# Kernel optimization log

Measured on AMD Instinct MI355X. Metric: run time of the kernel, lower is better.

## Reference

```python
import jax, jax.numpy as jnp
import numpy as np

N, E = 50000, 800000
DIN, DH, DOUT, HEADS = 128, 128, 128, 4
NEG_SLOPE = 0.2
LN_EPS = 1e-5


def setup_inputs() -> dict:
    key = jax.random.key(0)
    ks = jax.random.split(key, 20)
    s = 0.05
    inp = {
        "x": jax.random.normal(ks[0], (N, DIN), jnp.float32),
        "edge_index": jax.random.randint(ks[1], (2, E), 0, N, jnp.int32),
        "W_in": jax.random.normal(ks[2], (DIN, DH), jnp.float32) * s,
        "b_in": jnp.zeros((DH,), jnp.float32),
        # GAT layer 0 (heads=4, concat)
        "W0": jax.random.normal(ks[3], (DH, DH), jnp.float32) * s,
        "as0": jax.random.normal(ks[4], (HEADS, DH // HEADS), jnp.float32) * s,
        "ad0": jax.random.normal(ks[5], (HEADS, DH // HEADS), jnp.float32) * s,
        "b0": jnp.zeros((DH,), jnp.float32),
        # GAT layer 1 (heads=4, concat)
        "W1": jax.random.normal(ks[6], (DH, DH), jnp.float32) * s,
        "as1": jax.random.normal(ks[7], (HEADS, DH // HEADS), jnp.float32) * s,
        "ad1": jax.random.normal(ks[8], (HEADS, DH // HEADS), jnp.float32) * s,
        "b1": jnp.zeros((DH,), jnp.float32),
        # GAT layer 2 (heads=1, no concat)
        "W2": jax.random.normal(ks[9], (DH, DOUT), jnp.float32) * s,
        "as2": jax.random.normal(ks[10], (1, DOUT), jnp.float32) * s,
        "ad2": jax.random.normal(ks[11], (1, DOUT), jnp.float32) * s,
        "b2": jnp.zeros((DOUT,), jnp.float32),
    }
    return inp


def layer_norm(x):
    mu = jnp.mean(x, -1, keepdims=True)
    var = jnp.var(x, -1, keepdims=True)
    return (x - mu) * jax.lax.rsqrt(var + LN_EPS)


def gat_conv(x, src, dst, W, a_src, a_dst, bias, heads, concat):
    # x: [N, D_in]; src/dst include self-loops
    n = x.shape[0]
    c = W.shape[1] // heads
    h = (x @ W).reshape(n, heads, c)                       # [N,H,C]
    al_s = jnp.sum(h * a_src[None], -1)                    # [N,H]
    al_d = jnp.sum(h * a_dst[None], -1)                    # [N,H]
    e = jax.nn.leaky_relu(al_s[src] + al_d[dst], NEG_SLOPE)  # [Etot,H]
    m = jax.ops.segment_max(e, dst, num_segments=n)
    ex = jnp.exp(e - m[dst])
    z = jax.ops.segment_sum(ex, dst, num_segments=n)
    alpha = ex / (z[dst] + 1e-16)                          # [Etot,H]
    out = jax.ops.segment_sum(h[src] * alpha[:, :, None], dst, num_segments=n)  # [N,H,C]
    out = out.reshape(n, heads * c) if concat else jnp.mean(out, 1)
    return out + bias


def reference(x, edge_index, W_in, b_in, W0, as0, ad0, b0,
              W1, as1, ad1, b1, W2, as2, ad2, b2):
    n = x.shape[0]
    loop = jnp.arange(n, dtype=edge_index.dtype)
    src = jnp.concatenate([edge_index[0], loop])  # PyG GATConv adds self-loops
    dst = jnp.concatenate([edge_index[1], loop])

    h = jax.nn.relu(x @ W_in + b_in)  # dropout is identity in eval mode

    res = h
    h = gat_conv(h, src, dst, W0, as0, ad0, b0, HEADS, True)
    h = layer_norm(jax.nn.elu(h) + res)

    res = h
    h = gat_conv(h, src, dst, W1, as1, ad1, b1, HEADS, True)
    h = layer_norm(jax.nn.elu(h) + res)

    h = gat_conv(h, src, dst, W2, as2, ad2, b2, 1, False)
    return layer_norm(h)
```

## Files before the change

### kernel.cpp

```cpp
#include <hip/hip_runtime.h>
#include <hip/hip_bf16.h>

typedef unsigned short ushort_t;
typedef unsigned int uint_t;
typedef __attribute__((ext_vector_type(8))) short short8;
typedef __attribute__((ext_vector_type(4))) float f32x4;

__device__ __forceinline__ ushort_t f2bf(float f) {
    uint_t u = __float_as_uint(f);
    uint_t r = (u + 0x7FFFu + ((u >> 16) & 1u)) >> 16;
    return (ushort_t)r;
}
__device__ __forceinline__ float bf2f_lo(uint_t u) { return __uint_as_float(u << 16); }
__device__ __forceinline__ float bf2f_hi(uint_t u) { return __uint_as_float(u & 0xffff0000u); }
__device__ __forceinline__ float bf2f_hi_fast(uint_t u) { return __uint_as_float(u); }

#define BSH 8
#define BCK 256
#define CSR_CAP 6144

__global__ void prep_kernel(const float* __restrict__ W_in,
                            const float* __restrict__ W0, const float* __restrict__ as0,
                            const float* __restrict__ ad0,
                            const float* __restrict__ W1, const float* __restrict__ as1,
                            const float* __restrict__ ad1,
                            const float* __restrict__ W2, const float* __restrict__ as2,
                            const float* __restrict__ ad2,
                            ushort_t* __restrict__ BfIn, ushort_t* __restrict__ Bf0,
                            ushort_t* __restrict__ Bf1, ushort_t* __restrict__ Bf2,
                            const int* __restrict__ ei, int* __restrict__ gcnt,
                            int E, int N, int NB) {
    __shared__ int hist[256];
    int b = blockIdx.x;
    if (b < 35) {
        const float *W, *a_s, *a_d;
        ushort_t* Bf;
        int H, NT, nt;
        if (b < 8)       { W = W_in; a_s = nullptr; a_d = nullptr; Bf = BfIn; H = 0; NT = 8; nt = b; }
        else if (b < 17) { W = W0; a_s = as0; a_d = ad0; Bf = Bf0; H = 4; NT = 9; nt = b - 8; }
        else if (b < 26) { W = W1; a_s = as1; a_d = ad1; Bf = Bf1; H = 4; NT = 9; nt = b - 17; }
        else             { W = W2; a_s = as2; a_d = ad2; Bf = Bf2; H = 1; NT = 9; nt = b - 26; }
        int l = threadIdx.x & 63;
        int ks = threadIdx.x >> 6;
        int kb = ks * 32 + (l >> 4) * 8;
        int col = l & 15;
        ushort_t v[8];
        if (nt < 8) {
#pragma unroll
            for (int j = 0; j < 8; ++j)
                v[j] = f2bf(W[(size_t)(kb + j) * 128 + nt * 16 + col]);
        } else {
#pragma unroll
            for (int j = 0; j < 8; ++j) {
                int k = kb + j;
                float s = 0.f;
                if (H == 4) {
                    if (col < 4) {
                        for (int c = 0; c < 32; ++c)
                            s += W[(size_t)k * 128 + col * 32 + c] * a_s[col * 32 + c];
                    } else if (col < 8) {
                        int h = col - 4;
                        for (int c = 0; c < 32; ++c)
                            s += W[(size_t)k * 128 + h * 32 + c] * a_d[h * 32 + c];
                    }
                } else {
                    if (col == 0) {
                        for (int c = 0; c < 128; ++c) s += W[(size_t)k * 128 + c] * a_s[c];
                    } else if (col == 1) {
                        for (int c = 0; c < 128; ++c) s += W[(size_t)k * 128 + c] * a_d[c];
                    }
                }
                v[j] = f2bf(s);
            }
        }
        uint4 u;
        u.x = (uint_t)v[0] | ((uint_t)v[1] << 16);
        u.y = (uint_t)v[2] | ((uint_t)v[3] << 16);
        u.z = (uint_t)v[4] | ((uint_t)v[5] << 16);
        u.w = (uint_t)v[6] | ((uint_t)v[7] << 16);
        *(uint4*)(Bf + ((size_t)(ks * NT + nt) * 64 + l) * 8) = u;
    } else {
        int tid = threadIdx.x;
        hist[tid] = 0;
        __syncthreads();
        int base = (b - 35) * 1024;
        int Etot = E + N;
#pragma unroll
        for (int r = 0; r < 4; ++r) {
            int i = base + r * 256 + tid;
            if (i < Etot) {
                int dst = (i < E) ? ei[E + i] : (i - E);
                atomicAdd(&hist[dst >> BSH], 1);
            }
        }
        __syncthreads();
        if (tid < NB && hist[tid]) atomicAdd(&gcnt[tid], hist[tid]);
    }
}

__global__ void bucket_base(const int* __restrict__ gcnt, int* __restrict__ gbase,
                            int* __restrict__ gcur, int* __restrict__ rowp,
                            int NB, int N, int Etot) {
    __shared__ int ws[4];
    int t = threadIdx.x, lane = t & 63, w = t >> 6;
    int v = (t < NB) ? gcnt[t] : 0;
    int x = v;
#pragma unroll
    for (int off = 1; off < 64; off <<= 1) {
        int t2 = __shfl_up(x, off, 64);
        if (lane >= off) x += t2;
    }
    if (lane == 63) ws[w] = x;
    __syncthreads();
    int add = 0;
    for (int j = 0; j < w; ++j) add += ws[j];
    int excl = add + x - v;
    if (t < NB) {
        gbase[t] = excl;
        gcur[t] = excl;
    }
    if (t == 0) {
        gbase[NB] = Etot;
        rowp[N] = Etot;
    }
}

__global__ void bucket_scatter(const int* __restrict__ ei, int* __restrict__ gcur,
                               uint2* __restrict__ pairs, int E, int N, int NB) {
    __shared__ int hist[256];
    __shared__ int bbase[256];
    __shared__ int cur[256];
    int tid = threadIdx.x;
    hist[tid] = 0;
    __syncthreads();
    int base = blockIdx.x * 1024;
    int Etot = E + N;
    int srcv[4], dstv[4], bk[4];
    bool val[4];
#pragma unroll
    for (int r = 0; r < 4; ++r) {
        int i = base + r * 256 + tid;
        val[r] = (i < Etot);
        if (val[r]) {
            srcv[r] = (i < E) ? ei[i] : (i - E);
            dstv[r] = (i < E) ? ei[E + i] : (i - E);
            bk[r] = dstv[r] >> BSH;
            atomicAdd(&hist[bk[r]], 1);
        }
    }
    __syncthreads();
    if (tid < NB && hist[tid]) bbase[tid] = atomicAdd(&gcur[tid], hist[tid]);
    cur[tid] = 0;
    __syncthreads();
#pragma unroll
    for (int r = 0; r < 4; ++r) {
        if (val[r]) {
            int pos = bbase[bk[r]] + atomicAdd(&cur[bk[r]], 1);
            uint2 p;
            p.x = (uint_t)srcv[r];
            p.y = (uint_t)dstv[r];
            pairs[pos] = p;
        }
    }
}

__global__ void bucket_csr(const uint2* __restrict__ pairs, const int* __restrict__ gbase,
                           int* __restrict__ rowp, int* __restrict__ csrc, int N) {
    __shared__ int cnt[256];
    __shared__ int ws[4];
    __shared__ int stage[CSR_CAP];
    int b = blockIdx.x, tid = threadIdx.x;
    int eBeg = gbase[b], eEnd = gbase[b + 1];
    int M = eEnd - eBeg;
    cnt[tid] = 0;
    __syncthreads();
    for (int t = tid; t < M; t += 256) {
        uint2 pr = pairs[eBeg + t];
        atomicAdd(&cnt[pr.y & (BCK - 1)], 1);
    }
    __syncthreads();
    int v = cnt[tid];
    int lane = tid & 63, w = tid >> 6;
    int x = v;
#pragma unroll
    for (int off = 1; off < 64; off <<= 1) {
        int t2 = __shfl_up(x, off, 64);
        if (lane >= off) x += t2;
    }
    if (lane == 63) ws[w] = x;
    __syncthreads();
    int add = 0;
    for (int j = 0; j < w; ++j) add += ws[j];
    int excl = add + x - v;
    int node = (b << BSH) + tid;
    if (node < N) rowp[node] = eBeg + excl;
    __syncthreads();
    cnt[tid] = excl;
    __syncthreads();
    for (int t = tid; t < M; t += 256) {
        uint2 pr = pairs[eBeg + t];
        int pos = atomicAdd(&cnt[pr.y & (BCK - 1)], 1);
        if (pos < CSR_CAP) stage[pos] = (int)pr.x;
        else csrc[eBeg + pos] = (int)pr.x;
    }
    __syncthreads();
    int lim = (M < CSR_CAP) ? M : CSR_CAP;
    for (int t = tid; t < lim; t += 256) csrc[eBeg + t] = stage[t];
}

template <int MODE>
__device__ __forceinline__ void gemm_epilogue(f32x4* acc, int r0, int lg, int lc,
                                              const float* bias, ushort_t* outB,
                                              float* alS, float* alD) {
    if (MODE == 0) {
#pragma unroll
        for (int r = 0; r < 4; ++r) {
            int row = r0 + lg * 4 + r;
            ushort_t* op = outB + (size_t)row * 128 + lc;
#pragma unroll
            for (int nt = 0; nt < 8; ++nt) {
                float v = fmaxf(acc[nt][r] + bias[nt * 16 + lc], 0.f);
                op[nt * 16] = f2bf(v);
            }
        }
    } else {
#pragma unroll
        for (int r = 0; r < 4; ++r) {
            int row = r0 + lg * 4 + r;
            ushort_t* op = outB + (size_t)row * 128 + lc;
#pragma unroll
            for (int nt = 0; nt < 8; ++nt) op[nt * 16] = f2bf(acc[nt][r]);
            float lv = acc[8][r];
            if (MODE == 1) {
                if (lc < 4) alS[(size_t)row * 4 + lc] = lv;
                else if (lc < 8) alD[(size_t)row * 4 + (lc - 4)] = lv;
            } else {
                if (lc == 0) alS[row] = lv;
                else if (lc == 1) alD[row] = lv;
            }
        }
    }
}

template <int MODE>
__launch_bounds__(256)
__global__ void gemm_mfma(const float* __restrict__ Af, const ushort_t* __restrict__ Ab,
                          const ushort_t* __restrict__ Bf, const float* __restrict__ bias,
                          ushort_t* __restrict__ outB, float* __restrict__ alS,
                          float* __restrict__ alD, int M) {
    const int NT = (MODE == 0) ? 8 : 9;
    __shared__ ushort_t Bs[4 * 9 * 64 * 8];
    {
        const int tot = 4 * NT * 64;
        for (int t = threadIdx.x; t < tot; t += 256)
            ((uint4*)Bs)[t] = ((const uint4*)Bf)[t];
    }
    __syncthreads();

    int wid = threadIdx.x >> 6, l = threadIdx.x & 63;
    int lg = l >> 4, lc = l & 15;
    int r0 = (blockIdx.x * 4 + wid) * 32;
    if (r0 >= M) return;
    bool has1 = (r0 + 16) < M;
    int rowA0 = r0 + lc;
    int rowA1 = has1 ? (r0 + 16 + lc) : rowA0;

    f32x4 acc0[9], acc1[9];
#pragma unroll
    for (int nt = 0; nt < NT; ++nt) {
        acc0[nt] = (f32x4){0.f, 0.f, 0.f, 0.f};
        acc1[nt] = (f32x4){0.f, 0.f, 0.f, 0.f};
    }

#pragma unroll
    for (int ks = 0; ks < 4; ++ks) {
        int k0 = ks * 32 + lg * 8;
        short8 af0, af1;
        if (MODE == 0) {
            const float* ap0 = Af + (size_t)rowA0 * 128 + k0;
            const float* ap1 = Af + (size_t)rowA1 * 128 + k0;
            float4 x0 = *(const float4*)ap0;
            float4 x1 = *(const float4*)(ap0 + 4);
            float4 y0 = *(const float4*)ap1;
            float4 y1 = *(const float4*)(ap1 + 4);
            af0[0] = (short)f2bf(x0.x); af0[1] = (short)f2bf(x0.y);
            af0[2] = (short)f2bf(x0.z); af0[3] = (short)f2bf(x0.w);
            af0[4] = (short)f2bf(x1.x); af0[5] = (short)f2bf(x1.y);
            af0[6] = (short)f2bf(x1.z); af0[7] = (short)f2bf(x1.w);
            af1[0] = (short)f2bf(y0.x); af1[1] = (short)f2bf(y0.y);
            af1[2] = (short)f2bf(y0.z); af1[3] = (short)f2bf(y0.w);
            af1[4] = (short)f2bf(y1.x); af1[5] = (short)f2bf(y1.y);
            af1[6] = (short)f2bf(y1.z); af1[7] = (short)f2bf(y1.w);
        } else {
            af0 = *(const short8*)(Ab + (size_t)rowA0 * 128 + k0);
            af1 = *(const short8*)(Ab + (size_t)rowA1 * 128 + k0);
        }
#pragma unroll
        for (int nt = 0; nt < NT; ++nt) {
            short8 bfr = *(const short8*)(Bs + ((size_t)(ks * NT + nt) * 64 + l) * 8);
            acc0[nt] = __builtin_amdgcn_mfma_f32_16x16x32_bf16(af0, bfr, acc0[nt], 0, 0, 0);
            acc1[nt] = __builtin_amdgcn_mfma_f32_16x16x32_bf16(af1, bfr, acc1[nt], 0, 0, 0);
        }
    }

    gemm_epilogue<MODE>(acc0, r0, lg, lc, bias, outB, alS, alD);
    if (has1) gemm_epilogue<MODE>(acc1, r0 + 16, lg, lc, bias, outB, alS, alD);
}

template <int H, int FINAL>
__launch_bounds__(256)
__global__ void gat_aggregate(const ushort_t* __restrict__ hWb,
                              const float* __restrict__ alS,
                              const float* __restrict__ alD,
                              const int* __restrict__ rowp,
                              const int* __restrict__ csrc,
                              const float* __restrict__ bias,
                              const ushort_t* __restrict__ resb,
                              ushort_t* __restrict__ outb,
                              float* __restrict__ outf, int n) {
    __shared__ float pbuf[4][64][4];
    __shared__ int obuf[4][64];
    int wid = threadIdx.x >> 6;
    int lane = threadIdx.x & 63;
    int node = blockIdx.x * 4 + wid;
    if (node >= n) return;
    int g = lane >> 4;
    int j = lane & 15;
    int hsel = (H == 4) ? (j >> 2) : 0;
    float ald[4];
    if (H == 4) {
        float4 t = *(const float4*)(alD + (size_t)node * 4);
        ald[0] = t.x; ald[1] = t.y; ald[2] = t.z; ald[3] = t.w;
    } else {
        ald[0] = alD[node];
    }
    int beg = rowp[node], end = rowp[node + 1];
    float zp0 = 0.f, zp1 = 0.f, zp2 = 0.f, zp3 = 0.f;
    float acc[8];
#pragma unroll
    for (int c = 0; c < 8; ++c) acc[c] = 0.f;
    const char* hbase = (const char*)hWb;
    int jo = j << 4;

    for (int base = beg; base < end; base += 64) {
        int nc = min(64, end - base);
        if (lane < nc) {
            int s = csrc[base + lane];
            obuf[wid][lane] = s << 8;
            if (H == 4) {
                float4 t = *(const float4*)(alS + (size_t)s * 4);
                float x0 = t.x + ald[0], x1 = t.y + ald[1];
                float x2 = t.z + ald[2], x3 = t.w + ald[3];
                x0 = (x0 > 0.f) ? x0 : 0.2f * x0;
                x1 = (x1 > 0.f) ? x1 : 0.2f * x1;
                x2 = (x2 > 0.f) ? x2 : 0.2f * x2;
                x3 = (x3 > 0.f) ? x3 : 0.2f * x3;
                float p0 = __expf(x0), p1 = __expf(x1);
                float p2 = __expf(x2), p3 = __expf(x3);
                zp0 += p0; zp1 += p1; zp2 += p2; zp3 += p3;
                float4 t4; t4.x = p0; t4.y = p1; t4.z = p2; t4.w = p3;
                *(float4*)&pbuf[wid][lane][0] = t4;
            } else {
                float x = alS[s] + ald[0];
                x = (x > 0.f) ? x : 0.2f * x;
                float p = __expf(x);
                zp0 += p;
                pbuf[wid][lane][0] = p;
            }
        } else {
            obuf[wid][lane] = node << 8;
            if (H == 4) {
                float4 t4; t4.x = 0.f; t4.y = 0.f; t4.z = 0.f; t4.w = 0.f;
                *(float4*)&pbuf[wid][lane][0] = t4;
            } else {
                pbuf[wid][lane][0] = 0.f;
            }
        }
        int padded = (nc + 7) & ~7;
        for (int i = 0; i < padded; i += 8) {
            int i0 = i + g, i1 = i + 4 + g;
            int o0 = obuf[wid][i0];
            int o1 = obuf[wid][i1];
            float p0 = pbuf[wid][i0][hsel];
            float p1 = pbuf[wid][i1][hsel];
            uint4 h0 = *(const uint4*)(hbase + o0 + jo);
            uint4 h1 = *(const uint4*)(hbase + o1 + jo);
            acc[0] += p0 * bf2f_lo(h0.x); acc[1] += p0 * bf2f_hi_fast(h0.x);
            acc[2] += p0 * bf2f_lo(h0.y); acc[3] += p0 * bf2f_hi_fast(h0.y);
            acc[4] += p0 * bf2f_lo(h0.z); acc[5] += p0 * bf2f_hi_fast(h0.z);
            acc[6] += p0 * bf2f_lo(h0.w); acc[7] += p0 * bf2f_hi_fast(h0.w);
            acc[0] += p1 * bf2f_lo(h1.x); acc[1] += p1 * bf2f_hi_fast(h1.x);
            acc[2] += p1 * bf2f_lo(h1.y); acc[3] += p1 * bf2f_hi_fast(h1.y);
            acc[4] += p1 * bf2f_lo(h1.z); acc[5] += p1 * bf2f_hi_fast(h1.z);
            acc[6] += p1 * bf2f_lo(h1.w); acc[7] += p1 * bf2f_hi_fast(h1.w);
        }
    }

#pragma unroll
    for (int c = 0; c < 8; ++c) {
        acc[c] += __shfl_xor(acc[c], 16, 64);
        acc[c] += __shfl_xor(acc[c], 32, 64);
    }
#pragma unroll
    for (int off = 1; off < 64; off <<= 1) {
        zp0 += __shfl_xor(zp0, off, 64);
        if (H == 4) {
            zp1 += __shfl_xor(zp1, off, 64);
            zp2 += __shfl_xor(zp2, off, 64);
            zp3 += __shfl_xor(zp3, off, 64);
        }
    }
    float zv;
    if (H == 1) zv = zp0;
    else zv = (hsel == 0) ? zp0 : (hsel == 1) ? zp1 : (hsel == 2) ? zp2 : zp3;
    float inv = 1.f / (zv + 1e-16f);

    int c0 = j * 8;
    const float4* bp = (const float4*)(bias + c0);
    float4 bv0 = bp[0], bv1 = bp[1];
    float val[8];
    val[0] = acc[0] * inv + bv0.x; val[1] = acc[1] * inv + bv0.y;
    val[2] = acc[2] * inv + bv0.z; val[3] = acc[3] * inv + bv0.w;
    val[4] = acc[4] * inv + bv1.x; val[5] = acc[5] * inv + bv1.y;
    val[6] = acc[6] * inv + bv1.z; val[7] = acc[7] * inv + bv1.w;
    if (!FINAL) {
        uint4 rv = *((const uint4*)(resb + ((size_t)node << 7)) + j);
        float rr[8] = {bf2f_lo(rv.x), bf2f_hi(rv.x), bf2f_lo(rv.y), bf2f_hi(rv.y),
                       bf2f_lo(rv.z), bf2f_hi(rv.z), bf2f_lo(rv.w), bf2f_hi(rv.w)};
#pragma unroll
        for (int c = 0; c < 8; ++c) {
            float vv = val[c];
            float ev = __expf(vv) - 1.f;
            val[c] = ((vv > 0.f) ? vv : ev) + rr[c];
        }
    }
    float s2 = 0.f;
#pragma unroll
    for (int c = 0; c < 8; ++c) s2 += val[c];
#pragma unroll
    for (int off = 1; off < 16; off <<= 1) s2 += __shfl_xor(s2, off, 64);
    float mean = s2 * (1.f / 128.f);
    float q = 0.f;
    float dd[8];
#pragma unroll
    for (int c = 0; c < 8; ++c) {
        dd[c] = val[c] - mean;
        q += dd[c] * dd[c];
    }
#pragma unroll
    for (int off = 1; off < 16; off <<= 1) q += __shfl_xor(q, off, 64);
    float r = rsqrtf(q * (1.f / 128.f) + 1e-5f);
    if (g == 0) {
        if (FINAL) {
            float* op = outf + ((size_t)node << 7) + c0;
            *(float4*)op = make_float4(dd[0] * r, dd[1] * r, dd[2] * r, dd[3] * r);
            *(float4*)(op + 4) = make_float4(dd[4] * r, dd[5] * r, dd[6] * r, dd[7] * r);
        } else {
            uint4 u;
            u.x = (uint_t)f2bf(dd[0] * r) | ((uint_t)f2bf(dd[1] * r) << 16);
            u.y = (uint_t)f2bf(dd[2] * r) | ((uint_t)f2bf(dd[3] * r) << 16);
            u.z = (uint_t)f2bf(dd[4] * r) | ((uint_t)f2bf(dd[5] * r) << 16);
            u.w = (uint_t)f2bf(dd[6] * r) | ((uint_t)f2bf(dd[7] * r) << 16);
            *((uint4*)(outb + ((size_t)node << 7)) + j) = u;
        }
    }
}

extern "C" void kernel_launch(void* const* d_in, const int* in_sizes, int n_in,
                              void* d_out, int out_size, void* d_ws, size_t ws_size,
                              hipStream_t stream) {
    const int N = in_sizes[0] / 128;
    const int E = in_sizes[1] / 2;
    const int Etot = E + N;
    const int NB = (N + BCK - 1) / BCK;

    const float* x    = (const float*)d_in[0];
    const int*   ei   = (const int*)d_in[1];
    const float* W_in = (const float*)d_in[2];
    const float* b_in = (const float*)d_in[3];
    const float* W0   = (const float*)d_in[4];
    const float* as0  = (const float*)d_in[5];
    const float* ad0  = (const float*)d_in[6];
    const float* b0   = (const float*)d_in[7];
    const float* W1   = (const float*)d_in[8];
    const float* as1  = (const float*)d_in[9];
    const float* ad1  = (const float*)d_in[10];
    const float* b1   = (const float*)d_in[11];
    const float* W2   = (const float*)d_in[12];
    const float* as2  = (const float*)d_in[13];
    const float* ad2  = (const float*)d_in[14];
    const float* b2   = (const float*)d_in[15];

    char* wsp = (char*)d_ws;
    size_t off = 0;
    auto carve = [&](size_t bytes) -> void* {
        void* p = wsp + off;
        off += (bytes + 255) & ~(size_t)255;
        return p;
    };
    ushort_t* hAb  = (ushort_t*)carve((size_t)N * 128 * 2);
    ushort_t* hBb  = (ushort_t*)carve((size_t)N * 128 * 2);
    ushort_t* hWb  = (ushort_t*)carve((size_t)N * 128 * 2);
    float*    alS  = (float*)carve((size_t)N * 4 * 4);
    float*    alD  = (float*)carve((size_t)N * 4 * 4);
    int*      rowp = (int*)carve((size_t)(N + 1) * 4);
    int*      csrc = (int*)carve((size_t)Etot * 4);
    int*      gcnt = (int*)carve((size_t)256 * 4);
    int*      gbase= (int*)carve((size_t)257 * 4);
    int*      gcur = (int*)carve((size_t)256 * 4);
    ushort_t* BfIn = (ushort_t*)carve((size_t)4 * 8 * 64 * 8 * 2);
    ushort_t* Bf0  = (ushort_t*)carve((size_t)4 * 9 * 64 * 8 * 2);
    ushort_t* Bf1  = (ushort_t*)carve((size_t)4 * 9 * 64 * 8 * 2);
    ushort_t* Bf2  = (ushort_t*)carve((size_t)4 * 9 * 64 * 8 * 2);
    uint2*    pairs = (uint2*)hWb;
    (void)ws_size; (void)n_in; (void)out_size;

    int gsc = (Etot + 1023) / 1024;

    hipMemsetAsync(gcnt, 0, 256 * 4, stream);
    prep_kernel<<<35 + gsc, 256, 0, stream>>>(W_in, W0, as0, ad0, W1, as1, ad1,
                                              W2, as2, ad2, BfIn, Bf0, Bf1, Bf2,
                                              ei, gcnt, E, N, NB);
    bucket_base<<<1, 256, 0, stream>>>(gcnt, gbase, gcur, rowp, NB, N, Etot);
    bucket_scatter<<<gsc, 256, 0, stream>>>(ei, gcur, pairs, E, N, NB);
    bucket_csr<<<NB, 256, 0, stream>>>(pairs, gbase, rowp, csrc, N);

    int gg = (N + 127) / 128;
    int ga = (N + 3) / 4;

    gemm_mfma<0><<<gg, 256, 0, stream>>>(x, nullptr, BfIn, b_in, hAb,
                                         nullptr, nullptr, N);
    gemm_mfma<1><<<gg, 256, 0, stream>>>(nullptr, hAb, Bf0, nullptr, hWb, alS, alD, N);
    gat_aggregate<4, 0><<<ga, 256, 0, stream>>>(hWb, alS, alD, rowp, csrc, b0,
                                                hAb, hBb, nullptr, N);
    gemm_mfma<1><<<gg, 256, 0, stream>>>(nullptr, hBb, Bf1, nullptr, hWb, alS, alD, N);
    gat_aggregate<4, 0><<<ga, 256, 0, stream>>>(hWb, alS, alD, rowp, csrc, b1,
                                                hBb, hAb, nullptr, N);
    gemm_mfma<2><<<gg, 256, 0, stream>>>(nullptr, hAb, Bf2, nullptr, hWb, alS, alD, N);
    gat_aggregate<1, 1><<<ga, 256, 0, stream>>>(hWb, alS, alD, rowp, csrc, b2,
                                                nullptr, nullptr, (float*)d_out, N);
}
```

Measured before the change: 247.2 us.

## Replace global atomic bucket offsets with per-block histogram scan for CSR build

The CSR bucketing now stores a histogram per block and runs a single-block scan that computes each block's offset into every bucket. Scatter then writes from precomputed offsets, with no global atomics, no recount of the histogram and no memset. Each block also covers 4096 edges instead of 1024, which cuts the block count. The cost is a serial loop over roughly 208 blocks in the one-block scan kernel and fewer, larger scatter blocks.

```diff
diff --git a/kernel.cpp b/kernel.cpp
--- a/kernel.cpp
+++ b/kernel.cpp
@@ -18,6 +18,7 @@
 #define BSH 8
 #define BCK 256
 #define CSR_CAP 6144
+#define EPB 4096
 
 __global__ void prep_kernel(const float* __restrict__ W_in,
                             const float* __restrict__ W0, const float* __restrict__ as0,
@@ -28,8 +29,8 @@
                             const float* __restrict__ ad2,
                             ushort_t* __restrict__ BfIn, ushort_t* __restrict__ Bf0,
                             ushort_t* __restrict__ Bf1, ushort_t* __restrict__ Bf2,
-                            const int* __restrict__ ei, int* __restrict__ gcnt,
-                            int E, int N, int NB) {
+                            const int* __restrict__ ei, int* __restrict__ bhist,
+                            int E, int N) {
     __shared__ int hist[256];
     int b = blockIdx.x;
     if (b < 35) {
@@ -81,12 +82,13 @@
         *(uint4*)(Bf + ((size_t)(ks * NT + nt) * 64 + l) * 8) = u;
     } else {
         int tid = threadIdx.x;
+        int blk = b - 35;
         hist[tid] = 0;
         __syncthreads();
-        int base = (b - 35) * 1024;
+        int base = blk * EPB;
         int Etot = E + N;
 #pragma unroll
-        for (int r = 0; r < 4; ++r) {
+        for (int r = 0; r < EPB / 256; ++r) {
             int i = base + r * 256 + tid;
             if (i < Etot) {
                 int dst = (i < E) ? ei[E + i] : (i - E);
@@ -94,17 +96,23 @@
             }
         }
         __syncthreads();
-        if (tid < NB && hist[tid]) atomicAdd(&gcnt[tid], hist[tid]);
-    }
-}
-
-__global__ void bucket_base(const int* __restrict__ gcnt, int* __restrict__ gbase,
-                            int* __restrict__ gcur, int* __restrict__ rowp,
-                            int NB, int N, int Etot) {
+        bhist[blk * 256 + tid] = hist[tid];
+    }
+}
+
+__global__ void csr_scan(const int* __restrict__ bhist, int* __restrict__ obase,
+                         int* __restrict__ gbase, int* __restrict__ rowp,
+                         int NBLK, int N, int Etot) {
     __shared__ int ws[4];
-    int t = threadIdx.x, lane = t & 63, w = t >> 6;
-    int v = (t < NB) ? gcnt[t] : 0;
-    int x = v;
+    int t = threadIdx.x;
+    int run = 0;
+    for (int blk = 0; blk < NBLK; ++blk) {
+        int v = bhist[blk * 256 + t];
+        obase[blk * 256 + t] = run;
+        run += v;
+    }
+    int lane = t & 63, w = t >> 6;
+    int x = run;
 #pragma unroll
     for (int off = 1; off < 64; off <<= 1) {
         int t2 = __shfl_up(x, off, 64);
@@ -114,51 +122,34 @@
     __syncthreads();
     int add = 0;
     for (int j = 0; j < w; ++j) add += ws[j];
-    int excl = add + x - v;
-    if (t < NB) {
-        gbase[t] = excl;
-        gcur[t] = excl;
-    }
+    int excl = add + x - run;
+    gbase[t] = excl;
     if (t == 0) {
-        gbase[NB] = Etot;
+        gbase[256] = Etot;
         rowp[N] = Etot;
     }
 }
 
-__global__ void bucket_scatter(const int* __restrict__ ei, int* __restrict__ gcur,
-                               uint2* __restrict__ pairs, int E, int N, int NB) {
-    __shared__ int hist[256];
-    __shared__ int bbase[256];
+__global__ void csr_scatter(const int* __restrict__ ei, const int* __restrict__ gbase,
+                            const int* __restrict__ obase, uint2* __restrict__ pairs,
+                            int E, int N) {
     __shared__ int cur[256];
     int tid = threadIdx.x;
-    hist[tid] = 0;
-    __syncthreads();
-    int base = blockIdx.x * 1024;
+    int blk = blockIdx.x;
+    cur[tid] = gbase[tid] + obase[blk * 256 + tid];
+    __syncthreads();
+    int base = blk * EPB;
     int Etot = E + N;
-    int srcv[4], dstv[4], bk[4];
-    bool val[4];
-#pragma unroll
-    for (int r = 0; r < 4; ++r) {
+#pragma unroll
+    for (int r = 0; r < EPB / 256; ++r) {
         int i = base + r * 256 + tid;
-        val[r] = (i < Etot);
-        if (val[r]) {
-            srcv[r] = (i < E) ? ei[i] : (i - E);
-            dstv[r] = (i < E) ? ei[E + i] : (i - E);
-            bk[r] = dstv[r] >> BSH;
-            atomicAdd(&hist[bk[r]], 1);
-        }
-    }
-    __syncthreads();
-    if (tid < NB && hist[tid]) bbase[tid] = atomicAdd(&gcur[tid], hist[tid]);
-    cur[tid] = 0;
-    __syncthreads();
-#pragma unroll
-    for (int r = 0; r < 4; ++r) {
-        if (val[r]) {
-            int pos = bbase[bk[r]] + atomicAdd(&cur[bk[r]], 1);
+        if (i < Etot) {
+            int src = (i < E) ? ei[i] : (i - E);
+            int dst = (i < E) ? ei[E + i] : (i - E);
+            int pos = atomicAdd(&cur[dst >> BSH], 1);
             uint2 p;
-            p.x = (uint_t)srcv[r];
-            p.y = (uint_t)dstv[r];
+            p.x = (uint_t)src;
+            p.y = (uint_t)dst;
             pairs[pos] = p;
         }
     }
@@ -473,6 +464,7 @@
     const int E = in_sizes[1] / 2;
     const int Etot = E + N;
     const int NB = (N + BCK - 1) / BCK;
+    const int NBLK = (Etot + EPB - 1) / EPB;
 
     const float* x    = (const float*)d_in[0];
     const int*   ei   = (const int*)d_in[1];
@@ -505,9 +497,9 @@
     float*    alD  = (float*)carve((size_t)N * 4 * 4);
     int*      rowp = (int*)carve((size_t)(N + 1) * 4);
     int*      csrc = (int*)carve((size_t)Etot * 4);
-    int*      gcnt = (int*)carve((size_t)256 * 4);
+    int*      bhist= (int*)carve((size_t)NBLK * 256 * 4);
+    int*      obase= (int*)carve((size_t)NBLK * 256 * 4);
     int*      gbase= (int*)carve((size_t)257 * 4);
-    int*      gcur = (int*)carve((size_t)256 * 4);
     ushort_t* BfIn = (ushort_t*)carve((size_t)4 * 8 * 64 * 8 * 2);
     ushort_t* Bf0  = (ushort_t*)carve((size_t)4 * 9 * 64 * 8 * 2);
     ushort_t* Bf1  = (ushort_t*)carve((size_t)4 * 9 * 64 * 8 * 2);
@@ -515,14 +507,11 @@
     uint2*    pairs = (uint2*)hWb;
     (void)ws_size; (void)n_in; (void)out_size;
 
-    int gsc = (Etot + 1023) / 1024;
-
-    hipMemsetAsync(gcnt, 0, 256 * 4, stream);
-    prep_kernel<<<35 + gsc, 256, 0, stream>>>(W_in, W0, as0, ad0, W1, as1, ad1,
-                                              W2, as2, ad2, BfIn, Bf0, Bf1, Bf2,
-                                              ei, gcnt, E, N, NB);
-    bucket_base<<<1, 256, 0, stream>>>(gcnt, gbase, gcur, rowp, NB, N, Etot);
-    bucket_scatter<<<gsc, 256, 0, stream>>>(ei, gcur, pairs, E, N, NB);
+    prep_kernel<<<35 + NBLK, 256, 0, stream>>>(W_in, W0, as0, ad0, W1, as1, ad1,
+                                               W2, as2, ad2, BfIn, Bf0, Bf1, Bf2,
+                                               ei, bhist, E, N);
+    csr_scan<<<1, 256, 0, stream>>>(bhist, obase, gbase, rowp, NBLK, N, Etot);
+    csr_scatter<<<NBLK, 256, 0, stream>>>(ei, gbase, obase, pairs, E, N);
     bucket_csr<<<NB, 256, 0, stream>>>(pairs, gbase, rowp, csrc, N);
 
     int gg = (N + 127) / 128;
```

Result: slower. 275.0 us (+11.2%).
